# Performance work log

Measured on AMD Instinct MI355X. Metric: run time of the kernel, lower is better.

## Reference

```python
import jax, jax.numpy as jnp
import numpy as np

E = 8            # moe_num_experts
FFN = 8192       # ffn_hidden_size
D = 2048         # d_model
B, T = 1, 4096


def setup_inputs() -> dict:
    key = jax.random.key(0)
    k1, k2, k3, k4 = jax.random.split(key, 4)
    x = jax.random.normal(k1, (B, T, D), dtype=jnp.float32)
    # params stored flat as (E*FFN, D), as in the flax module
    w1 = jax.random.normal(k2, (E * FFN, D), dtype=jnp.float32) * 0.02
    v1 = jax.random.normal(k3, (E * FFN, D), dtype=jnp.float32) * 0.02
    w2 = jax.random.normal(k4, (E * FFN, D), dtype=jnp.float32) * 0.02
    return {"x": x, "w1": w1, "v1": v1, "w2": w2, "expert_idx": 3}


def reference(x, w1, v1, w2, expert_idx):
    # select this expert's weight slabs: (FFN, D) each
    expert_shape = (E, FFN, D)
    ew1 = w1.reshape(expert_shape)[expert_idx]
    ev1 = v1.reshape(expert_shape)[expert_idx]
    ew2 = w2.reshape(expert_shape)[expert_idx]
    # gate and up projections: [B,T,D] x [D,FFN] -> [B,T,FFN]
    x1 = jnp.einsum('btd,fd->btf', x, ew1)
    x2 = jnp.einsum('btd,fd->btf', x, ev1)
    h = jax.nn.silu(x1) * x2
    # down projection (note: matmul with ew2, i.e. contraction over FFN)
    out = jnp.einsum('btf,fd->btd', h, ew2)
    return out
```

## Files before the change

kernel.cpp:

```cpp
#include <hip/hip_runtime.h>

#define E_NUM 8
#define FFN_DIM 8192
#define D_DIM 2048
#define T_DIM 4096

using bf16x8 = __attribute__((ext_vector_type(8))) short;
using f32x4  = __attribute__((ext_vector_type(4))) float;
using u16x8  = __attribute__((ext_vector_type(8))) unsigned short;

__device__ __forceinline__ unsigned short f2bf(float f) {
  union { float f; unsigned int u; } v; v.f = f;
  unsigned int u = v.u;
  unsigned int r = (u + 0x7FFFu + ((u >> 16) & 1u)) >> 16;
  return (unsigned short)r;
}

__device__ __forceinline__ void gload16(const unsigned short* g, const unsigned short* l) {
  __builtin_amdgcn_global_load_lds(
      (const __attribute__((address_space(1))) void*)g,
      (__attribute__((address_space(3))) void*)l, 16, 0, 0);
}

__global__ void convert_kernel(const float* __restrict__ src_base,
                               const int* __restrict__ eidx, long slab,
                               unsigned short* __restrict__ dst, long n) {
  const float* src = src_base + (long)(*eidx) * slab;
  long stride = (long)gridDim.x * blockDim.x;
  for (long i = (long)blockIdx.x * blockDim.x + threadIdx.x; i * 8 < n; i += stride) {
    long e = i * 8;
    const float4* p = (const float4*)(src + e);
    float4 f0 = p[0], f1 = p[1];
    u16x8 o;
    o[0] = f2bf(f0.x); o[1] = f2bf(f0.y); o[2] = f2bf(f0.z); o[3] = f2bf(f0.w);
    o[4] = f2bf(f1.x); o[5] = f2bf(f1.y); o[6] = f2bf(f1.z); o[7] = f2bf(f1.w);
    *(u16x8*)(dst + e) = o;
  }
}

__global__ void transpose_kernel(const float* __restrict__ w2,
                                 const int* __restrict__ eidx,
                                 unsigned short* __restrict__ dst) {
  __shared__ unsigned short tile[32][33];
  const float* src = w2 + (long)(*eidx) * (long)FFN_DIM * D_DIM;
  int d0 = blockIdx.x << 5;
  int f0 = blockIdx.y << 5;
  int tx = threadIdx.x & 31, ty = threadIdx.x >> 5;
#pragma unroll
  for (int i = 0; i < 4; ++i) {
    int f = ty + i * 8;
    tile[f][tx] = f2bf(src[(long)(f0 + f) * D_DIM + d0 + tx]);
  }
  __syncthreads();
#pragma unroll
  for (int i = 0; i < 4; ++i) {
    int d = ty + i * 8;
    dst[(long)(d0 + d) * FFN_DIM + f0 + tx] = tile[tx][d];
  }
}

__global__ __launch_bounds__(512, 2) void gemm1_silu(
    const unsigned short* __restrict__ Xb,
    const unsigned short* __restrict__ W1b,
    const unsigned short* __restrict__ V1b,
    unsigned short* __restrict__ Hb) {
  __shared__ __align__(16) unsigned short sA[2 * 256 * 64];
  __shared__ __align__(16) unsigned short sB1[2 * 128 * 64];
  __shared__ __align__(16) unsigned short sB2[2 * 128 * 64];

  const int tid = threadIdx.x;
  const int wv = tid >> 6, l = tid & 63;
  const int wm = wv >> 1, wn = wv & 1;
  const int kq = l >> 4, lr = l & 15;
  const int m0 = blockIdx.y << 8;
  const int n0 = blockIdx.x << 7;

  const int rsub = tid >> 3;
  const int sslot8 = ((tid & 7) ^ ((tid >> 3) & 7)) << 3;
  const unsigned short* gA0  = Xb  + (long)(m0 + rsub) * D_DIM + sslot8;
  const unsigned short* gB1r = W1b + (long)(n0 + rsub) * D_DIM + sslot8;
  const unsigned short* gB2r = V1b + (long)(n0 + rsub) * D_DIM + sslot8;

#define ST_A(r_)  gload16(gA0  + (long)((r_) * 64) * D_DIM + tc, sA  + sb * 16384 + (r_) * 4096 + wv * 512)
#define ST_B1(r_) gload16(gB1r + (long)((r_) * 64) * D_DIM + tc, sB1 + sb * 8192  + (r_) * 4096 + wv * 512)
#define ST_B2(r_) gload16(gB2r + (long)((r_) * 64) * D_DIM + tc, sB2 + sb * 8192  + (r_) * 4096 + wv * 512)
#define VMCNT2 asm volatile("s_waitcnt vmcnt(2)" ::: "memory")
#define VMCNT0 asm volatile("s_waitcnt vmcnt(0)" ::: "memory")
#define BAR __builtin_amdgcn_s_barrier()

  int raoff[4], rboff[4];
#pragma unroll
  for (int m = 0; m < 4; ++m) {
    int row = wm * 64 + m * 16 + lr;
    raoff[m] = row * 64 + ((kq ^ (row & 7)) << 3);
  }
#pragma unroll
  for (int n = 0; n < 4; ++n) {
    int row = wn * 64 + n * 16 + lr;
    rboff[n] = row * 64 + ((kq ^ (row & 7)) << 3);
  }

  f32x4 acc1[4][4], acc2[4][4];
  f32x4 z = {0.f, 0.f, 0.f, 0.f};
#pragma unroll
  for (int m = 0; m < 4; ++m)
#pragma unroll
    for (int n = 0; n < 4; ++n) { acc1[m][n] = z; acc2[m][n] = z; }

  {
    int tc = 0, sb = 0;
    ST_A(0); ST_A(1); ST_A(2); ST_A(3);
    ST_B1(0); ST_B1(1); ST_B2(0); ST_B2(1);
    VMCNT2;
    BAR;
  }

  const int NT = D_DIM / 64;
  for (int t = 0; t < NT; ++t) {
    const int db = t & 1;
    const unsigned short* Ab  = sA  + db * 16384;
    const unsigned short* B1b = sB1 + db * 8192;
    const unsigned short* B2b = sB2 + db * 8192;
    const int pf = (t < NT - 1);
    const int tc = (t + 1) << 6;
    const int sb = db ^ 1;
    bf16x8 af[4], bf_[4];

#pragma unroll
    for (int m = 0; m < 4; ++m) af[m] = *(const bf16x8*)(Ab + raoff[m]);
#pragma unroll
    for (int n = 0; n < 4; ++n) bf_[n] = *(const bf16x8*)(B1b + rboff[n]);
    if (pf) { ST_A(0); ST_A(1); }
    BAR;
    __builtin_amdgcn_s_setprio(1);
#pragma unroll
    for (int m = 0; m < 4; ++m)
#pragma unroll
      for (int n = 0; n < 4; ++n)
        acc1[m][n] = __builtin_amdgcn_mfma_f32_16x16x32_bf16(af[m], bf_[n], acc1[m][n], 0, 0, 0);
    __builtin_amdgcn_s_setprio(0);
    if (pf) { VMCNT2; } else { VMCNT0; }
    BAR;

#pragma unroll
    for (int n = 0; n < 4; ++n) bf_[n] = *(const bf16x8*)(B2b + rboff[n]);
    if (pf) { ST_A(2); ST_A(3); }
    BAR;
    __builtin_amdgcn_s_setprio(1);
#pragma unroll
    for (int m = 0; m < 4; ++m)
#pragma unroll
      for (int n = 0; n < 4; ++n)
        acc2[m][n] = __builtin_amdgcn_mfma_f32_16x16x32_bf16(af[m], bf_[n], acc2[m][n], 0, 0, 0);
    __builtin_amdgcn_s_setprio(0);
    BAR;

#pragma unroll
    for (int m = 0; m < 4; ++m) af[m] = *(const bf16x8*)(Ab + (raoff[m] ^ 32));
#pragma unroll
    for (int n = 0; n < 4; ++n) bf_[n] = *(const bf16x8*)(B1b + (rboff[n] ^ 32));
    if (pf) { ST_B1(0); ST_B1(1); }
    BAR;
    __builtin_amdgcn_s_setprio(1);
#pragma unroll
    for (int m = 0; m < 4; ++m)
#pragma unroll
      for (int n = 0; n < 4; ++n)
        acc1[m][n] = __builtin_amdgcn_mfma_f32_16x16x32_bf16(af[m], bf_[n], acc1[m][n], 0, 0, 0);
    __builtin_amdgcn_s_setprio(0);
    BAR;

#pragma unroll
    for (int n = 0; n < 4; ++n) bf_[n] = *(const bf16x8*)(B2b + (rboff[n] ^ 32));
    if (pf) { ST_B2(0); ST_B2(1); }
    BAR;
    __builtin_amdgcn_s_setprio(1);
#pragma unroll
    for (int m = 0; m < 4; ++m)
#pragma unroll
      for (int n = 0; n < 4; ++n)
        acc2[m][n] = __builtin_amdgcn_mfma_f32_16x16x32_bf16(af[m], bf_[n], acc2[m][n], 0, 0, 0);
    __builtin_amdgcn_s_setprio(0);
    if (pf) { VMCNT2; }
    BAR;
  }

#pragma unroll
  for (int m = 0; m < 4; ++m)
#pragma unroll
    for (int n = 0; n < 4; ++n)
#pragma unroll
      for (int r = 0; r < 4; ++r) {
        int row = m0 + wm * 64 + m * 16 + kq * 4 + r;
        int col = n0 + wn * 64 + n * 16 + lr;
        float x1 = acc1[m][n][r], x2 = acc2[m][n][r];
        float hv = x1 / (1.f + __expf(-x1)) * x2;
        Hb[(long)row * FFN_DIM + col] = f2bf(hv);
      }
#undef ST_A
#undef ST_B1
#undef ST_B2
}

__global__ __launch_bounds__(256) void gemm2(
    const unsigned short* __restrict__ Hb,
    const unsigned short* __restrict__ W2T,
    float* __restrict__ out) {
  __shared__ __align__(16) unsigned short sA[128 * 32];
  __shared__ __align__(16) unsigned short sB[128 * 32];

  const int tid = threadIdx.x;
  const int w = tid >> 6, l = tid & 63;
  const int m0 = blockIdx.y << 7;
  const int n0 = blockIdx.x << 7;
  const int wm = w >> 1, wn = w & 1;
  const int kq = l >> 4, lr = l & 15;

  f32x4 z = {0.f, 0.f, 0.f, 0.f};
  f32x4 acc[4][4];
#pragma unroll
  for (int m = 0; m < 4; ++m)
#pragma unroll
    for (int n = 0; n < 4; ++n) acc[m][n] = z;

  const int colg = (l & 3) * 8;
  const int rsub = l >> 2;
  const unsigned short* gA0 = Hb + (long)(m0 + (w * 2 + 0) * 16 + rsub) * FFN_DIM + colg;
  const unsigned short* gA1 = Hb + (long)(m0 + (w * 2 + 1) * 16 + rsub) * FFN_DIM + colg;
  const unsigned short* gB0 = W2T + (long)(n0 + (w * 2 + 0) * 16 + rsub) * FFN_DIM + colg;
  const unsigned short* gB1 = W2T + (long)(n0 + (w * 2 + 1) * 16 + rsub) * FFN_DIM + colg;
  unsigned short* lA0 = sA + (w * 2 + 0) * 512;
  unsigned short* lA1 = sA + (w * 2 + 1) * 512;
  unsigned short* lB0 = sB + (w * 2 + 0) * 512;
  unsigned short* lB1 = sB + (w * 2 + 1) * 512;

  for (int k0 = 0; k0 < FFN_DIM; k0 += 32) {
    if (k0) __syncthreads();
    gload16(gA0 + k0, lA0);
    gload16(gA1 + k0, lA1);
    gload16(gB0 + k0, lB0);
    gload16(gB1 + k0, lB1);
    __syncthreads();

    const bf16x8* pA = (const bf16x8*)sA;
    const bf16x8* pB = (const bf16x8*)sB;
    bf16x8 a[4], b[4];
#pragma unroll
    for (int m = 0; m < 4; ++m) a[m] = pA[(wm * 64 + m * 16 + lr) * 4 + kq];
#pragma unroll
    for (int n = 0; n < 4; ++n) b[n] = pB[(wn * 64 + n * 16 + lr) * 4 + kq];
#pragma unroll
    for (int m = 0; m < 4; ++m)
#pragma unroll
      for (int n = 0; n < 4; ++n)
        acc[m][n] = __builtin_amdgcn_mfma_f32_16x16x32_bf16(a[m], b[n], acc[m][n], 0, 0, 0);
  }

#pragma unroll
  for (int m = 0; m < 4; ++m)
#pragma unroll
    for (int n = 0; n < 4; ++n)
#pragma unroll
      for (int r = 0; r < 4; ++r) {
        int row = m0 + wm * 64 + m * 16 + kq * 4 + r;
        int col = n0 + wn * 64 + n * 16 + lr;
        out[(long)row * D_DIM + col] = acc[m][n][r];
      }
}

extern "C" void kernel_launch(void* const* d_in, const int* in_sizes, int n_in,
                              void* d_out, int out_size, void* d_ws, size_t ws_size,
                              hipStream_t stream) {
  const float* x  = (const float*)d_in[0];
  const float* w1 = (const float*)d_in[1];
  const float* v1 = (const float*)d_in[2];
  const float* w2 = (const float*)d_in[3];
  const int* eidx = (const int*)d_in[4];

  char* ws = (char*)d_ws;
  unsigned short* Xb  = (unsigned short*)(ws);
  unsigned short* W1b = (unsigned short*)(ws + (16l << 20));
  unsigned short* V1b = (unsigned short*)(ws + (48l << 20));
  unsigned short* W2T = (unsigned short*)(ws + (80l << 20));
  unsigned short* Hb  = (unsigned short*)(ws + (112l << 20));
  float* out = (float*)d_out;

  long slab = (long)FFN_DIM * D_DIM;
  convert_kernel<<<2048, 256, 0, stream>>>(x,  eidx, 0,    Xb,  (long)T_DIM * D_DIM);
  convert_kernel<<<2048, 256, 0, stream>>>(w1, eidx, slab, W1b, slab);
  convert_kernel<<<2048, 256, 0, stream>>>(v1, eidx, slab, V1b, slab);
  transpose_kernel<<<dim3(D_DIM / 32, FFN_DIM / 32), 256, 0, stream>>>(w2, eidx, W2T);
  gemm1_silu<<<dim3(FFN_DIM / 128, T_DIM / 256), 512, 0, stream>>>(Xb, W1b, V1b, Hb);
  gemm2<<<dim3(D_DIM / 128, T_DIM / 128), 256, 0, stream>>>(Hb, W2T, out);
}
```

Measured before the change: 502.4 us.

## Rewrite gemm2 with 256x128 tiles and triple-buffered async loads; front-load gemm1 prefetch

gemm2 moves from a 128x128 tile with single-buffered LDS, 32-wide K steps and two syncs per step to a 512-thread, 256x128 tile kernel. It uses 64-wide K steps, XOR-swizzled LDS and a 3-stage global-to-LDS pipeline that prefetches two tiles ahead. This hides global memory latency and cuts the number of barriers per FLOP. gemm1 now issues all next-tile prefetches at the start of each iteration instead of spreading them across the four sub-phases, with the wait counts adjusted to match. Risks include higher LDS use in gemm2, which may limit occupancy, and a wait-count schedule that is easy to get wrong.

```diff
diff --git a/kernel.cpp b/kernel.cpp
--- a/kernel.cpp
+++ b/kernel.cpp
@@ -59,6 +59,12 @@
   }
 }
 
+#define VMCNT8 asm volatile("s_waitcnt vmcnt(8)" ::: "memory")
+#define VMCNT6 asm volatile("s_waitcnt vmcnt(6)" ::: "memory")
+#define VMCNT2 asm volatile("s_waitcnt vmcnt(2)" ::: "memory")
+#define VMCNT0 asm volatile("s_waitcnt vmcnt(0)" ::: "memory")
+#define BAR __builtin_amdgcn_s_barrier()
+
 __global__ __launch_bounds__(512, 2) void gemm1_silu(
     const unsigned short* __restrict__ Xb,
     const unsigned short* __restrict__ W1b,
@@ -84,9 +90,6 @@
 #define ST_A(r_)  gload16(gA0  + (long)((r_) * 64) * D_DIM + tc, sA  + sb * 16384 + (r_) * 4096 + wv * 512)
 #define ST_B1(r_) gload16(gB1r + (long)((r_) * 64) * D_DIM + tc, sB1 + sb * 8192  + (r_) * 4096 + wv * 512)
 #define ST_B2(r_) gload16(gB2r + (long)((r_) * 64) * D_DIM + tc, sB2 + sb * 8192  + (r_) * 4096 + wv * 512)
-#define VMCNT2 asm volatile("s_waitcnt vmcnt(2)" ::: "memory")
-#define VMCNT0 asm volatile("s_waitcnt vmcnt(0)" ::: "memory")
-#define BAR __builtin_amdgcn_s_barrier()
 
   int raoff[4], rboff[4];
 #pragma unroll
@@ -130,7 +133,10 @@
     for (int m = 0; m < 4; ++m) af[m] = *(const bf16x8*)(Ab + raoff[m]);
 #pragma unroll
     for (int n = 0; n < 4; ++n) bf_[n] = *(const bf16x8*)(B1b + rboff[n]);
-    if (pf) { ST_A(0); ST_A(1); }
+    if (pf) {
+      ST_A(0); ST_A(1); ST_A(2); ST_A(3);
+      ST_B1(0); ST_B1(1); ST_B2(0); ST_B2(1);
+    }
     BAR;
     __builtin_amdgcn_s_setprio(1);
 #pragma unroll
@@ -139,12 +145,11 @@
       for (int n = 0; n < 4; ++n)
         acc1[m][n] = __builtin_amdgcn_mfma_f32_16x16x32_bf16(af[m], bf_[n], acc1[m][n], 0, 0, 0);
     __builtin_amdgcn_s_setprio(0);
-    if (pf) { VMCNT2; } else { VMCNT0; }
+    if (pf) { VMCNT8; } else { VMCNT0; }
     BAR;
 
 #pragma unroll
     for (int n = 0; n < 4; ++n) bf_[n] = *(const bf16x8*)(B2b + rboff[n]);
-    if (pf) { ST_A(2); ST_A(3); }
     BAR;
     __builtin_amdgcn_s_setprio(1);
 #pragma unroll
@@ -159,7 +164,6 @@
     for (int m = 0; m < 4; ++m) af[m] = *(const bf16x8*)(Ab + (raoff[m] ^ 32));
 #pragma unroll
     for (int n = 0; n < 4; ++n) bf_[n] = *(const bf16x8*)(B1b + (rboff[n] ^ 32));
-    if (pf) { ST_B1(0); ST_B1(1); }
     BAR;
     __builtin_amdgcn_s_setprio(1);
 #pragma unroll
@@ -172,7 +176,6 @@
 
 #pragma unroll
     for (int n = 0; n < 4; ++n) bf_[n] = *(const bf16x8*)(B2b + (rboff[n] ^ 32));
-    if (pf) { ST_B2(0); ST_B2(1); }
     BAR;
     __builtin_amdgcn_s_setprio(1);
 #pragma unroll
@@ -202,58 +205,99 @@
 #undef ST_B2
 }
 
-__global__ __launch_bounds__(256) void gemm2(
+__global__ __launch_bounds__(512, 2) void gemm2(
     const unsigned short* __restrict__ Hb,
     const unsigned short* __restrict__ W2T,
     float* __restrict__ out) {
-  __shared__ __align__(16) unsigned short sA[128 * 32];
-  __shared__ __align__(16) unsigned short sB[128 * 32];
+  __shared__ __align__(16) unsigned short sA[3 * 256 * 64];
+  __shared__ __align__(16) unsigned short sB[3 * 128 * 64];
 
   const int tid = threadIdx.x;
-  const int w = tid >> 6, l = tid & 63;
-  const int m0 = blockIdx.y << 7;
+  const int wv = tid >> 6, l = tid & 63;
+  const int wm = wv >> 1, wn = wv & 1;
+  const int kq = l >> 4, lr = l & 15;
+  const int m0 = blockIdx.y << 8;
   const int n0 = blockIdx.x << 7;
-  const int wm = w >> 1, wn = w & 1;
-  const int kq = l >> 4, lr = l & 15;
-
+
+  const int rsub = tid >> 3;
+  const int sslot8 = ((tid & 7) ^ ((tid >> 3) & 7)) << 3;
+  const unsigned short* gA0  = Hb  + (long)(m0 + rsub) * FFN_DIM + sslot8;
+  const unsigned short* gB0r = W2T + (long)(n0 + rsub) * FFN_DIM + sslot8;
+
+#define ST2_A(r_) gload16(gA0  + (long)((r_) * 64) * FFN_DIM + tc2, sA + bwr * 16384 + (r_) * 4096 + wv * 512)
+#define ST2_B(r_) gload16(gB0r + (long)((r_) * 64) * FFN_DIM + tc2, sB + bwr * 8192  + (r_) * 4096 + wv * 512)
+
+  int raoff[4], rboff[4];
+#pragma unroll
+  for (int m = 0; m < 4; ++m) {
+    int row = wm * 64 + m * 16 + lr;
+    raoff[m] = row * 64 + ((kq ^ (row & 7)) << 3);
+  }
+#pragma unroll
+  for (int n = 0; n < 4; ++n) {
+    int row = wn * 64 + n * 16 + lr;
+    rboff[n] = row * 64 + ((kq ^ (row & 7)) << 3);
+  }
+
+  f32x4 acc[4][4];
   f32x4 z = {0.f, 0.f, 0.f, 0.f};
-  f32x4 acc[4][4];
 #pragma unroll
   for (int m = 0; m < 4; ++m)
 #pragma unroll
     for (int n = 0; n < 4; ++n) acc[m][n] = z;
 
-  const int colg = (l & 3) * 8;
-  const int rsub = l >> 2;
-  const unsigned short* gA0 = Hb + (long)(m0 + (w * 2 + 0) * 16 + rsub) * FFN_DIM + colg;
-  const unsigned short* gA1 = Hb + (long)(m0 + (w * 2 + 1) * 16 + rsub) * FFN_DIM + colg;
-  const unsigned short* gB0 = W2T + (long)(n0 + (w * 2 + 0) * 16 + rsub) * FFN_DIM + colg;
-  const unsigned short* gB1 = W2T + (long)(n0 + (w * 2 + 1) * 16 + rsub) * FFN_DIM + colg;
-  unsigned short* lA0 = sA + (w * 2 + 0) * 512;
-  unsigned short* lA1 = sA + (w * 2 + 1) * 512;
-  unsigned short* lB0 = sB + (w * 2 + 0) * 512;
-  unsigned short* lB1 = sB + (w * 2 + 1) * 512;
-
-  for (int k0 = 0; k0 < FFN_DIM; k0 += 32) {
-    if (k0) __syncthreads();
-    gload16(gA0 + k0, lA0);
-    gload16(gA1 + k0, lA1);
-    gload16(gB0 + k0, lB0);
-    gload16(gB1 + k0, lB1);
-    __syncthreads();
-
-    const bf16x8* pA = (const bf16x8*)sA;
-    const bf16x8* pB = (const bf16x8*)sB;
-    bf16x8 a[4], b[4];
-#pragma unroll
-    for (int m = 0; m < 4; ++m) a[m] = pA[(wm * 64 + m * 16 + lr) * 4 + kq];
-#pragma unroll
-    for (int n = 0; n < 4; ++n) b[n] = pB[(wn * 64 + n * 16 + lr) * 4 + kq];
-#pragma unroll
-    for (int m = 0; m < 4; ++m)
-#pragma unroll
-      for (int n = 0; n < 4; ++n)
-        acc[m][n] = __builtin_amdgcn_mfma_f32_16x16x32_bf16(a[m], b[n], acc[m][n], 0, 0, 0);
+  {
+    int tc2 = 0, bwr = 0;
+    ST2_A(0); ST2_A(1); ST2_A(2); ST2_A(3); ST2_B(0); ST2_B(1);
+    tc2 = 64; bwr = 1;
+    ST2_A(0); ST2_A(1); ST2_A(2); ST2_A(3); ST2_B(0); ST2_B(1);
+    VMCNT6;
+    BAR;
+  }
+
+  const int NT = FFN_DIM / 64;
+  int brd = 0;
+  for (int t = 0; t < NT; ++t) {
+    const unsigned short* Ab = sA + brd * 16384;
+    const unsigned short* Bb = sB + brd * 8192;
+    const int pf2 = (t + 2 < NT);
+    const int tc2 = (t + 2) << 6;
+    const int bwr = (brd + 2 >= 3) ? brd - 1 : brd + 2;
+    bf16x8 af[4], bf_[4];
+
+#pragma unroll
+    for (int m = 0; m < 4; ++m) af[m] = *(const bf16x8*)(Ab + raoff[m]);
+#pragma unroll
+    for (int n = 0; n < 4; ++n) bf_[n] = *(const bf16x8*)(Bb + rboff[n]);
+    if (pf2) {
+      ST2_A(0); ST2_A(1); ST2_A(2); ST2_A(3); ST2_B(0); ST2_B(1);
+    }
+    BAR;
+    __builtin_amdgcn_s_setprio(1);
+#pragma unroll
+    for (int m = 0; m < 4; ++m)
+#pragma unroll
+      for (int n = 0; n < 4; ++n)
+        acc[m][n] = __builtin_amdgcn_mfma_f32_16x16x32_bf16(af[m], bf_[n], acc[m][n], 0, 0, 0);
+    __builtin_amdgcn_s_setprio(0);
+    BAR;
+
+#pragma unroll
+    for (int m = 0; m < 4; ++m) af[m] = *(const bf16x8*)(Ab + (raoff[m] ^ 32));
+#pragma unroll
+    for (int n = 0; n < 4; ++n) bf_[n] = *(const bf16x8*)(Bb + (rboff[n] ^ 32));
+    BAR;
+    __builtin_amdgcn_s_setprio(1);
+#pragma unroll
+    for (int m = 0; m < 4; ++m)
+#pragma unroll
+      for (int n = 0; n < 4; ++n)
+        acc[m][n] = __builtin_amdgcn_mfma_f32_16x16x32_bf16(af[m], bf_[n], acc[m][n], 0, 0, 0);
+    __builtin_amdgcn_s_setprio(0);
+    if (pf2) { VMCNT6; } else if (t + 1 < NT) { VMCNT0; }
+    BAR;
+
+    brd = (brd + 1 == 3) ? 0 : brd + 1;
   }
 
 #pragma unroll
@@ -266,6 +310,8 @@
         int col = n0 + wn * 64 + n * 16 + lr;
         out[(long)row * D_DIM + col] = acc[m][n][r];
       }
+#undef ST2_A
+#undef ST2_B
 }
 
 extern "C" void kernel_launch(void* const* d_in, const int* in_sizes, int n_in,
@@ -291,5 +337,5 @@
   convert_kernel<<<2048, 256, 0, stream>>>(v1, eidx, slab, V1b, slab);
   transpose_kernel<<<dim3(D_DIM / 32, FFN_DIM / 32), 256, 0, stream>>>(w2, eidx, W2T);
   gemm1_silu<<<dim3(FFN_DIM / 128, T_DIM / 256), 512, 0, stream>>>(Xb, W1b, V1b, Hb);
-  gemm2<<<dim3(D_DIM / 128, T_DIM / 128), 256, 0, stream>>>(Hb, W2T, out);
-}
+  gemm2<<<dim3(D_DIM / 128, T_DIM / 256), 512, 0, stream>>>(Hb, W2T, out);
+}
```

New measurement: 538.4 us. 7.1% more time.
